# Kernel optimization log

Measured on AMD Instinct MI355X. Metric: run time of the kernel, lower is better.

Reference implementation:

```python
import jax, jax.numpy as jnp
import numpy as np

B = 65536      # bs * n_agents
N_AL = 9       # allies
N_EN = 10      # enemies
D_OWN = 96     # wrapped own obs dim (own + id + compact last action)
D_AL = 64      # ally feature dim
D_EN = 65      # enemy feature dim (+1 attack flag)
H = 4          # heads
A = 32         # attn_embed_dim per head
D = 32         # entity_embed_dim per head


def setup_inputs() -> dict:
    key = jax.random.key(0)
    ks = jax.random.split(key, 16)
    s = lambda fan_in: 1.0 / np.sqrt(fan_in)
    return {
        "own_obs": jax.random.normal(ks[0], (B, D_OWN), jnp.float32),
        "ally_feats": jax.random.normal(ks[1], (B, N_AL, D_AL), jnp.float32),
        "enemy_feats": jax.random.normal(ks[2], (B, N_EN, D_EN), jnp.float32),
        "Wq": jax.random.normal(ks[3], (D_OWN, A * H), jnp.float32) * s(D_OWN),
        "bq": jnp.zeros((A * H,), jnp.float32),
        "Wak": jax.random.normal(ks[4], (D_AL, A * H), jnp.float32) * s(D_AL),
        "bak": jnp.zeros((A * H,), jnp.float32),
        "Wav": jax.random.normal(ks[5], (D_AL, D * H), jnp.float32) * s(D_AL),
        "bav": jnp.zeros((D * H,), jnp.float32),
        "Wek": jax.random.normal(ks[6], (D_EN, A * H), jnp.float32) * s(D_EN),
        "bek": jnp.zeros((A * H,), jnp.float32),
        "Wev": jax.random.normal(ks[7], (D_EN, D * H), jnp.float32) * s(D_EN),
        "bev": jnp.zeros((D * H,), jnp.float32),
        "Wown": jax.random.normal(ks[8], (D_OWN, D * H), jnp.float32) * s(D_OWN),
        "bown": jnp.zeros((D * H,), jnp.float32),
    }


def _mha(q, k, v):
    # q: [B,H,A], k: [B,E,H,A], v: [B,E,H,D] -> [B, H*D]
    scale = jnp.asarray(1.0 / np.sqrt(A), q.dtype)
    energy = jnp.einsum("bha,beha->bhe", q, k) * scale
    score = jax.nn.softmax(energy, axis=-1)
    out = jnp.einsum("bhe,behd->bhd", score, v)
    return out.reshape(out.shape[0], H * D)


def reference(own_obs, ally_feats, enemy_feats, Wq, bq, Wak, bak, Wav, bav,
              Wek, bek, Wev, bev, Wown, bown):
    own_feature = own_obs @ Wown + bown                                   # [B, H*D]
    q = (own_obs @ Wq + bq).reshape(B, H, A)                              # [B,H,A]
    ally_k = (ally_feats @ Wak + bak).reshape(B, N_AL, H, A)
    ally_v = (ally_feats @ Wav + bav).reshape(B, N_AL, H, D)
    enemy_k = (enemy_feats @ Wek + bek).reshape(B, N_EN, H, A)
    enemy_v = (enemy_feats @ Wev + bev).reshape(B, N_EN, H, D)
    ally_feature = _mha(q, ally_k, ally_v)                                # [B, H*D]
    enemy_feature = _mha(q, enemy_k, enemy_v)                             # [B, H*D]
    attn_feature = jnp.concatenate([own_feature, ally_feature, enemy_feature], axis=-1)
    return attn_feature                                                   # [B, 3*H*D]
```

## Files before the change

kernel.cpp:

```cpp
#include <hip/hip_runtime.h>
#include <hip/hip_bf16.h>
#include <stdint.h>

#define N_AL 9
#define N_EN 10
#define D_OWN 96
#define D_AL 64
#define D_EN 65
#define BROWS 65536

#define WS_P0 0
#define WS_B0 49152
#define WS_P1 50176
#define WS_P2 87040
#define REGION 36864

#define QSCALE (0.17677669529663688f * 1.4426950408889634f)

typedef __attribute__((ext_vector_type(8))) short short8;
typedef __attribute__((ext_vector_type(4))) float f32x4;
typedef __attribute__((ext_vector_type(4), aligned(4))) float f32x4u;
typedef __attribute__((address_space(1))) const unsigned guint;
typedef __attribute__((address_space(3))) unsigned luint;

static __device__ __forceinline__ unsigned cvtpk(float lo, float hi) {
    unsigned r;
    asm("v_cvt_pk_bf16_f32 %0, %1, %2" : "=v"(r) : "v"(lo), "v"(hi));
    return r;
}
static __device__ __forceinline__ float bflo(unsigned u) { return __builtin_bit_cast(float, u << 16); }
static __device__ __forceinline__ float bfhi(unsigned u) { return __builtin_bit_cast(float, u & 0xffff0000u); }

static __device__ __forceinline__ short8 pack8(f32x4 a, f32x4 b) {
    union { unsigned u[4]; short8 s; } t;
    t.u[0] = cvtpk(a[0], a[1]); t.u[1] = cvtpk(a[2], a[3]);
    t.u[2] = cvtpk(b[0], b[1]); t.u[3] = cvtpk(b[2], b[3]);
    return t.s;
}
static __device__ __forceinline__ short f2bf1(float x) { return (short)(cvtpk(x, 0.0f) & 0xffffu); }

template <int CTRL>
static __device__ __forceinline__ float dpp_mov(float x) {
    return __builtin_bit_cast(float,
        __builtin_amdgcn_update_dpp(0, __builtin_bit_cast(int, x), CTRL, 0xf, 0xf, true));
}
static __device__ __forceinline__ float reduce16(float x) {
    x += dpp_mov<0xB1>(x);
    x += dpp_mov<0x4E>(x);
    x += dpp_mov<0x141>(x);
    x += dpp_mov<0x140>(x);
    return x;
}

__global__ void pack_weights(const float* __restrict__ Wq,  const float* __restrict__ bq,
                             const float* __restrict__ Wak, const float* __restrict__ Wav,
                             const float* __restrict__ bav, const float* __restrict__ Wek,
                             const float* __restrict__ Wev, const float* __restrict__ bev,
                             const float* __restrict__ Wown,const float* __restrict__ bown,
                             char* __restrict__ ws)
{
    int id = blockIdx.x * 256 + threadIdx.x;
    if (id < 7168) {
        const float *W0, *W1; int KS; short* dst; int f; bool isP0 = false;
        if (id < 3072)      { W0 = Wq;  W1 = Wown; KS = 3; dst = (short*)(ws + WS_P0); f = id; isP0 = true; }
        else if (id < 5120) { W0 = Wak; W1 = Wav;  KS = 2; dst = (short*)(ws + WS_P1); f = id - 3072; }
        else                { W0 = Wek; W1 = Wev;  KS = 2; dst = (short*)(ws + WS_P2); f = id - 5120; }
        int lane = f & 63, ks = (f >> 6) % KS, tile = f / (KS * 64);
        int col = tile * 16 + (lane & 15), k0 = ks * 32 + (lane >> 4) * 8;
        const float* W = (col < 128) ? W0 : W1;
        float scl = (isP0 && col < 128) ? QSCALE : 1.0f;
        int c = col & 127;
        short8 v;
        #pragma unroll
        for (int i = 0; i < 8; ++i) v[i] = f2bf1(W[(k0 + i) * 128 + c] * scl);
        *(short8*)(dst + (size_t)f * 8) = v;
    } else if (id < 7936) {
        int j = id - 7168;
        float* b0  = (float*)(ws + WS_B0);
        float* bV1 = (float*)(ws + WS_P1 + 32768);
        float* w64 = (float*)(ws + WS_P2 + 32768);
        float* bV2 = (float*)(ws + WS_P2 + 33792);
        if      (j < 128) b0[j] = bq[j] * QSCALE;
        else if (j < 256) b0[j] = bown[j - 128];
        else if (j < 384) w64[j - 256] = Wek[64 * 128 + (j - 256)];
        else if (j < 512) w64[j - 256] = Wev[64 * 128 + (j - 384)];
        else if (j < 640) bV1[j - 512] = bav[j - 512];
        else              bV2[j - 640] = bev[j - 640];
    }
}

static __device__ __forceinline__ void stage36(const char* src, char* smem, int wid, int lane) {
    #pragma unroll
    for (int c = 0; c < 9; ++c) {
        int off = (wid * 9 + c) * 1024;
        __builtin_amdgcn_global_load_lds((guint*)(src + off + lane * 16),
                                         (luint*)(smem + off), 16, 0, 0);
    }
}

static __device__ __forceinline__ void loadAllyRaw(const float* __restrict__ ally,
                                                   int arow, int kgrp, int e, f32x4* v) {
    const float* ap = ally + ((size_t)arow * N_AL + e) * D_AL + kgrp * 8;
    v[0] = *(const f32x4*)(ap);
    v[1] = *(const f32x4*)(ap + 4);
    v[2] = *(const f32x4*)(ap + 32);
    v[3] = *(const f32x4*)(ap + 36);
}

static __device__ __forceinline__ void loadEnemyRaw(const float* __restrict__ enemy,
                                                    int arow, int row0, int kgrp, int e,
                                                    f32x4* v, float* x64) {
    const float* ap = enemy + ((size_t)arow * N_EN + e) * D_EN + kgrp * 8;
    v[0] = *(const f32x4u*)(ap);
    v[1] = *(const f32x4u*)(ap + 4);
    v[2] = *(const f32x4u*)(ap + 32);
    v[3] = *(const f32x4u*)(ap + 36);
    #pragma unroll
    for (int r = 0; r < 4; ++r)
        x64[r] = enemy[((size_t)(row0 + kgrp * 4 + r) * N_EN + e) * D_EN + 64];
}

template <bool X64>
static __device__ __forceinline__ void entity_step(
    const short8* afr, const float* x64, const unsigned* qq,
    float (&accn)[2][4][4], float (&accd4)[4], const float (&hm)[4],
    const short* bpk, const float* w64lds, int lane)
{
    const int lrow = lane & 15;
    #pragma unroll
    for (int hp = 0; hp < 2; ++hp) {
        f32x4 acc4[4];
        #pragma unroll
        for (int j = 0; j < 4; ++j) {
            if (X64) {
                float w = w64lds[(4 * hp + j) * 16 + lrow];
                #pragma unroll
                for (int r = 0; r < 4; ++r) acc4[j][r] = x64[r] * w;
            } else {
                #pragma unroll
                for (int r = 0; r < 4; ++r) acc4[j][r] = 0.0f;
            }
        }
        #pragma unroll
        for (int ks = 0; ks < 2; ++ks)
            #pragma unroll
            for (int j = 0; j < 4; ++j) {
                short8 bfr = *(const short8*)(bpk + (size_t)(((4 * hp + j) * 2 + ks) * 64 + lane) * 8);
                acc4[j] = __builtin_amdgcn_mfma_f32_16x16x32_bf16(afr[ks], bfr, acc4[j], 0, 0, 0);
            }
        float p0[4], p1[4];
        #pragma unroll
        for (int r = 0; r < 4; ++r) { p0[r] = 0.0f; p1[r] = 0.0f; }
        #pragma unroll
        for (int j = 0; j < 4; ++j) {
            int t = 4 * hp + j;
            float* pp = (j < 2) ? p0 : p1;
            #pragma unroll
            for (int pr = 0; pr < 2; ++pr) {
                unsigned u = qq[t * 2 + pr];
                pp[2 * pr]     += bflo(u) * acc4[j][2 * pr];
                pp[2 * pr + 1] += bfhi(u) * acc4[j][2 * pr + 1];
            }
        }
        float s0[4], s1[4];
        #pragma unroll
        for (int r = 0; r < 4; ++r) {
            s0[r] = __builtin_amdgcn_exp2f(reduce16(p0[r]));
            s1[r] = __builtin_amdgcn_exp2f(reduce16(p1[r]));
            accd4[r] += hm[2 * hp] * s0[r] + hm[2 * hp + 1] * s1[r];
        }
        #pragma unroll
        for (int j = 0; j < 4; ++j) {
            if (X64) {
                float w = w64lds[128 + (4 * hp + j) * 16 + lrow];
                #pragma unroll
                for (int r = 0; r < 4; ++r) acc4[j][r] = x64[r] * w;
            } else {
                #pragma unroll
                for (int r = 0; r < 4; ++r) acc4[j][r] = 0.0f;
            }
        }
        #pragma unroll
        for (int ks = 0; ks < 2; ++ks)
            #pragma unroll
            for (int j = 0; j < 4; ++j) {
                short8 bfr = *(const short8*)(bpk + (size_t)(((8 + 4 * hp + j) * 2 + ks) * 64 + lane) * 8);
                acc4[j] = __builtin_amdgcn_mfma_f32_16x16x32_bf16(afr[ks], bfr, acc4[j], 0, 0, 0);
            }
        #pragma unroll
        for (int j = 0; j < 4; ++j) {
            const float* s = (j < 2) ? s0 : s1;
            #pragma unroll
            for (int r = 0; r < 4; ++r) accn[hp][j][r] += s[r] * acc4[j][r];
        }
    }
}

static __device__ __forceinline__ void write_attn(float* __restrict__ out, int row0, int kgrp,
                                                  int lrow, int coloff,
                                                  const float (&accn)[2][4][4],
                                                  const float (&accd4)[4],
                                                  const float* bVlds)
{
    float inv[4][4];
    #pragma unroll
    for (int r = 0; r < 4; ++r) {
        inv[0][r] = __builtin_amdgcn_rcpf(dpp_mov<0x00>(accd4[r]));
        inv[1][r] = __builtin_amdgcn_rcpf(dpp_mov<0x55>(accd4[r]));
        inv[2][r] = __builtin_amdgcn_rcpf(dpp_mov<0xAA>(accd4[r]));
        inv[3][r] = __builtin_amdgcn_rcpf(dpp_mov<0xFF>(accd4[r]));
    }
    #pragma unroll
    for (int hp = 0; hp < 2; ++hp)
        #pragma unroll
        for (int j = 0; j < 4; ++j) {
            int col = (4 * hp + j) * 16 + lrow;
            float bb = bVlds[col];
            #pragma unroll
            for (int r = 0; r < 4; ++r)
                out[(size_t)(row0 + kgrp * 4 + r) * 384 + coloff + col] =
                    accn[hp][j][r] * inv[2 * hp + (j >> 1)][r] + bb;
        }
}

__global__ __launch_bounds__(256, 4)
void TrSFRNNAgent_fused(const float* __restrict__ own,
                        const float* __restrict__ ally,
                        const float* __restrict__ enemy,
                        const char* __restrict__ ws,
                        float* __restrict__ out)
{
    __shared__ __align__(16) char smem[REGION];
    const int tid = threadIdx.x, lane = tid & 63, wid = tid >> 6;
    const int row0 = blockIdx.x * 64 + wid * 16;
    const int lrow = lane & 15, kgrp = lane >> 4;
    const int arow = row0 + lrow;
    float hm[4];
    #pragma unroll
    for (int h = 0; h < 4; ++h) hm[h] = ((lane & 3) == h) ? 1.0f : 0.0f;

    stage36(ws + WS_P1, smem, wid, lane);

    f32x4 prefA[4];
    loadAllyRaw(ally, arow, kgrp, 0, prefA);

    unsigned qq[16];
    {
        short8 afr0[3];
        {
            const float* ap = own + (size_t)arow * D_OWN + kgrp * 8;
            #pragma unroll
            for (int ks = 0; ks < 3; ++ks) {
                f32x4 a = *(const f32x4*)(ap + ks * 32);
                f32x4 b = *(const f32x4*)(ap + ks * 32 + 4);
                afr0[ks] = pack8(a, b);
            }
        }
        const short* bp0 = (const short*)(ws + WS_P0);
        const float* b0  = (const float*)(ws + WS_B0);
        #pragma unroll
        for (int pass = 0; pass < 2; ++pass) {
            f32x4 acc[8];
            #pragma unroll
            for (int t = 0; t < 8; ++t)
                #pragma unroll
                for (int r = 0; r < 4; ++r) acc[t][r] = 0.0f;
            #pragma unroll
            for (int ks = 0; ks < 3; ++ks)
                #pragma unroll
                for (int t = 0; t < 8; ++t) {
                    short8 bfr = *(const short8*)(bp0 + (size_t)(((pass * 8 + t) * 3 + ks) * 64 + lane) * 8);
                    acc[t] = __builtin_amdgcn_mfma_f32_16x16x32_bf16(afr0[ks], bfr, acc[t], 0, 0, 0);
                }
            if (pass == 0) {
                #pragma unroll
                for (int t = 0; t < 8; ++t) {
                    float bb = b0[t * 16 + lrow];
                    qq[t * 2]     = cvtpk(acc[t][0] + bb, acc[t][1] + bb);
                    qq[t * 2 + 1] = cvtpk(acc[t][2] + bb, acc[t][3] + bb);
                }
            } else {
                #pragma unroll
                for (int t = 0; t < 8; ++t) {
                    float bb = b0[128 + t * 16 + lrow];
                    #pragma unroll
                    for (int r = 0; r < 4; ++r)
                        out[(size_t)(row0 + kgrp * 4 + r) * 384 + t * 16 + lrow] = acc[t][r] + bb;
                }
            }
        }
    }
    __syncthreads();

    f32x4 prefE[4]; float x64e[4];
    {
        float accn[2][4][4] = {{{0}}}; float accd4[4] = {0, 0, 0, 0};
        #pragma unroll 1
        for (int e = 0; e < N_AL; ++e) {
            short8 afr[2];
            afr[0] = pack8(prefA[0], prefA[1]);
            afr[1] = pack8(prefA[2], prefA[3]);
            if (e + 1 < N_AL) loadAllyRaw(ally, arow, kgrp, e + 1, prefA);
            entity_step<false>(afr, nullptr, qq, accn, accd4, hm, (const short*)smem, nullptr, lane);
        }
        loadEnemyRaw(enemy, arow, row0, kgrp, 0, prefE, x64e);
        write_attn(out, row0, kgrp, lrow, 128, accn, accd4, (const float*)(smem + 32768));
    }
    __syncthreads();
    stage36(ws + WS_P2, smem, wid, lane);
    __syncthreads();

    {
        const float* w64lds = (const float*)(smem + 32768);
        float accn[2][4][4] = {{{0}}}; float accd4[4] = {0, 0, 0, 0};
        #pragma unroll 1
        for (int e = 0; e < N_EN; ++e) {
            short8 afr[2];
            afr[0] = pack8(prefE[0], prefE[1]);
            afr[1] = pack8(prefE[2], prefE[3]);
            float xc[4];
            #pragma unroll
            for (int r = 0; r < 4; ++r) xc[r] = x64e[r];
            if (e + 1 < N_EN) loadEnemyRaw(enemy, arow, row0, kgrp, e + 1, prefE, x64e);
            entity_step<true>(afr, xc, qq, accn, accd4, hm, (const short*)smem, w64lds, lane);
        }
        write_attn(out, row0, kgrp, lrow, 256, accn, accd4, (const float*)(smem + 33792));
    }
}

extern "C" void kernel_launch(void* const* d_in, const int* in_sizes, int n_in,
                              void* d_out, int out_size, void* d_ws, size_t ws_size,
                              hipStream_t stream)
{
    (void)in_sizes; (void)n_in; (void)out_size; (void)ws_size;
    const float* own   = (const float*)d_in[0];
    const float* ally  = (const float*)d_in[1];
    const float* enemy = (const float*)d_in[2];
    const float* Wq    = (const float*)d_in[3];
    const float* bq    = (const float*)d_in[4];
    const float* Wak   = (const float*)d_in[5];
    const float* Wav   = (const float*)d_in[7];
    const float* bav   = (const float*)d_in[8];
    const float* Wek   = (const float*)d_in[9];
    const float* Wev   = (const float*)d_in[11];
    const float* bev   = (const float*)d_in[12];
    const float* Wown  = (const float*)d_in[13];
    const float* bown  = (const float*)d_in[14];

    pack_weights<<<31, 256, 0, stream>>>(Wq, bq, Wak, Wav, bav, Wek, Wev, bev, Wown, bown,
                                         (char*)d_ws);
    TrSFRNNAgent_fused<<<BROWS / 64, 256, 0, stream>>>(own, ally, enemy,
                                                       (const char*)d_ws, (float*)d_out);
}
```

Measured before the change: 153.1 us.

## Hold K/V weight fragments in registers instead of staging through LDS

Removes the LDS staging of the ally and enemy K/V weight fragments and their block barriers. Each wave now loads all 32 bf16 B-fragments straight into registers once per phase and reuses them across every entity. The rank-1 term from the 65th enemy feature in the V projection is pulled out of the per-entity loop. It becomes a softmax-weighted scalar sum applied once at output time. Launch bounds drop from 4 to 2 blocks per SM so the larger register footprint fits, which trades occupancy for fewer LDS reads and syncs.

```diff
diff --git a/kernel.cpp b/kernel.cpp
--- a/kernel.cpp
+++ b/kernel.cpp
@@ -13,15 +13,12 @@
 #define WS_B0 49152
 #define WS_P1 50176
 #define WS_P2 87040
-#define REGION 36864
 
 #define QSCALE (0.17677669529663688f * 1.4426950408889634f)
 
 typedef __attribute__((ext_vector_type(8))) short short8;
 typedef __attribute__((ext_vector_type(4))) float f32x4;
 typedef __attribute__((ext_vector_type(4), aligned(4))) float f32x4u;
-typedef __attribute__((address_space(1))) const unsigned guint;
-typedef __attribute__((address_space(3))) unsigned luint;
 
 static __device__ __forceinline__ unsigned cvtpk(float lo, float hi) {
     unsigned r;
@@ -89,15 +86,6 @@
     }
 }
 
-static __device__ __forceinline__ void stage36(const char* src, char* smem, int wid, int lane) {
-    #pragma unroll
-    for (int c = 0; c < 9; ++c) {
-        int off = (wid * 9 + c) * 1024;
-        __builtin_amdgcn_global_load_lds((guint*)(src + off + lane * 16),
-                                         (luint*)(smem + off), 16, 0, 0);
-    }
-}
-
 static __device__ __forceinline__ void loadAllyRaw(const float* __restrict__ ally,
                                                    int arow, int kgrp, int e, f32x4* v) {
     const float* ap = ally + ((size_t)arow * N_AL + e) * D_AL + kgrp * 8;
@@ -122,35 +110,39 @@
 
 template <bool X64>
 static __device__ __forceinline__ void entity_step(
-    const short8* afr, const float* x64, const unsigned* qq,
-    float (&accn)[2][4][4], float (&accd4)[4], const float (&hm)[4],
-    const short* bpk, const float* w64lds, int lane)
-{
-    const int lrow = lane & 15;
+    const short8 (&afr)[2], const short8 (&BK)[16], const short8 (&BV)[16],
+    const unsigned* qq, float (&accn)[2][4][4], float (&accd4)[4], float (&SX)[4],
+    const float* x64, const float* w64K, int lane3)
+{
     #pragma unroll
     for (int hp = 0; hp < 2; ++hp) {
-        f32x4 acc4[4];
+        f32x4 kacc[4], vacc[4];
         #pragma unroll
         for (int j = 0; j < 4; ++j) {
             if (X64) {
-                float w = w64lds[(4 * hp + j) * 16 + lrow];
-                #pragma unroll
-                for (int r = 0; r < 4; ++r) acc4[j][r] = x64[r] * w;
+                float w = w64K[4 * hp + j];
+                #pragma unroll
+                for (int r = 0; r < 4; ++r) kacc[j][r] = x64[r] * w;
             } else {
                 #pragma unroll
-                for (int r = 0; r < 4; ++r) acc4[j][r] = 0.0f;
+                for (int r = 0; r < 4; ++r) kacc[j][r] = 0.0f;
             }
         }
         #pragma unroll
         for (int ks = 0; ks < 2; ++ks)
             #pragma unroll
-            for (int j = 0; j < 4; ++j) {
-                short8 bfr = *(const short8*)(bpk + (size_t)(((4 * hp + j) * 2 + ks) * 64 + lane) * 8);
-                acc4[j] = __builtin_amdgcn_mfma_f32_16x16x32_bf16(afr[ks], bfr, acc4[j], 0, 0, 0);
-            }
-        float p0[4], p1[4];
-        #pragma unroll
-        for (int r = 0; r < 4; ++r) { p0[r] = 0.0f; p1[r] = 0.0f; }
+            for (int j = 0; j < 4; ++j)
+                kacc[j] = __builtin_amdgcn_mfma_f32_16x16x32_bf16(afr[ks], BK[(4 * hp + j) * 2 + ks], kacc[j], 0, 0, 0);
+        #pragma unroll
+        for (int j = 0; j < 4; ++j)
+            #pragma unroll
+            for (int r = 0; r < 4; ++r) vacc[j][r] = 0.0f;
+        #pragma unroll
+        for (int ks = 0; ks < 2; ++ks)
+            #pragma unroll
+            for (int j = 0; j < 4; ++j)
+                vacc[j] = __builtin_amdgcn_mfma_f32_16x16x32_bf16(afr[ks], BV[(4 * hp + j) * 2 + ks], vacc[j], 0, 0, 0);
+        float p0[4] = {0, 0, 0, 0}, p1[4] = {0, 0, 0, 0};
         #pragma unroll
         for (int j = 0; j < 4; ++j) {
             int t = 4 * hp + j;
@@ -158,8 +150,8 @@
             #pragma unroll
             for (int pr = 0; pr < 2; ++pr) {
                 unsigned u = qq[t * 2 + pr];
-                pp[2 * pr]     += bflo(u) * acc4[j][2 * pr];
-                pp[2 * pr + 1] += bfhi(u) * acc4[j][2 * pr + 1];
+                pp[2 * pr]     += bflo(u) * kacc[j][2 * pr];
+                pp[2 * pr + 1] += bfhi(u) * kacc[j][2 * pr + 1];
             }
         }
         float s0[4], s1[4];
@@ -167,40 +159,27 @@
         for (int r = 0; r < 4; ++r) {
             s0[r] = __builtin_amdgcn_exp2f(reduce16(p0[r]));
             s1[r] = __builtin_amdgcn_exp2f(reduce16(p1[r]));
-            accd4[r] += hm[2 * hp] * s0[r] + hm[2 * hp + 1] * s1[r];
-        }
-        #pragma unroll
-        for (int j = 0; j < 4; ++j) {
-            if (X64) {
-                float w = w64lds[128 + (4 * hp + j) * 16 + lrow];
-                #pragma unroll
-                for (int r = 0; r < 4; ++r) acc4[j][r] = x64[r] * w;
-            } else {
-                #pragma unroll
-                for (int r = 0; r < 4; ++r) acc4[j][r] = 0.0f;
-            }
-        }
-        #pragma unroll
-        for (int ks = 0; ks < 2; ++ks)
-            #pragma unroll
-            for (int j = 0; j < 4; ++j) {
-                short8 bfr = *(const short8*)(bpk + (size_t)(((8 + 4 * hp + j) * 2 + ks) * 64 + lane) * 8);
-                acc4[j] = __builtin_amdgcn_mfma_f32_16x16x32_bf16(afr[ks], bfr, acc4[j], 0, 0, 0);
-            }
+            accd4[r] += (lane3 == 2 * hp ? s0[r] : 0.0f) + (lane3 == 2 * hp + 1 ? s1[r] : 0.0f);
+            if (X64)
+                SX[r] += (lane3 == 2 * hp ? s0[r] * x64[r] : 0.0f)
+                       + (lane3 == 2 * hp + 1 ? s1[r] * x64[r] : 0.0f);
+        }
         #pragma unroll
         for (int j = 0; j < 4; ++j) {
             const float* s = (j < 2) ? s0 : s1;
             #pragma unroll
-            for (int r = 0; r < 4; ++r) accn[hp][j][r] += s[r] * acc4[j][r];
-        }
-    }
-}
-
+            for (int r = 0; r < 4; ++r) accn[hp][j][r] += s[r] * vacc[j][r];
+        }
+    }
+}
+
+template <bool X64>
 static __device__ __forceinline__ void write_attn(float* __restrict__ out, int row0, int kgrp,
                                                   int lrow, int coloff,
                                                   const float (&accn)[2][4][4],
-                                                  const float (&accd4)[4],
-                                                  const float* bVlds)
+                                                  const float (&accd4)[4], const float (&SX)[4],
+                                                  const float* __restrict__ bV,
+                                                  const float* __restrict__ w64V)
 {
     float inv[4][4];
     #pragma unroll
@@ -210,36 +189,44 @@
         inv[2][r] = __builtin_amdgcn_rcpf(dpp_mov<0xAA>(accd4[r]));
         inv[3][r] = __builtin_amdgcn_rcpf(dpp_mov<0xFF>(accd4[r]));
     }
+    float sxh[4][4];
+    if (X64) {
+        #pragma unroll
+        for (int r = 0; r < 4; ++r) {
+            sxh[0][r] = dpp_mov<0x00>(SX[r]);
+            sxh[1][r] = dpp_mov<0x55>(SX[r]);
+            sxh[2][r] = dpp_mov<0xAA>(SX[r]);
+            sxh[3][r] = dpp_mov<0xFF>(SX[r]);
+        }
+    }
     #pragma unroll
     for (int hp = 0; hp < 2; ++hp)
         #pragma unroll
         for (int j = 0; j < 4; ++j) {
             int col = (4 * hp + j) * 16 + lrow;
-            float bb = bVlds[col];
-            #pragma unroll
-            for (int r = 0; r < 4; ++r)
-                out[(size_t)(row0 + kgrp * 4 + r) * 384 + coloff + col] =
-                    accn[hp][j][r] * inv[2 * hp + (j >> 1)][r] + bb;
-        }
-}
-
-__global__ __launch_bounds__(256, 4)
+            int h = 2 * hp + (j >> 1);
+            float bb = bV[col];
+            float wv = X64 ? w64V[col] : 0.0f;
+            #pragma unroll
+            for (int r = 0; r < 4; ++r) {
+                float a = accn[hp][j][r] + (X64 ? sxh[h][r] * wv : 0.0f);
+                out[(size_t)(row0 + kgrp * 4 + r) * 384 + coloff + col] = a * inv[h][r] + bb;
+            }
+        }
+}
+
+__global__ __launch_bounds__(256, 2)
 void TrSFRNNAgent_fused(const float* __restrict__ own,
                         const float* __restrict__ ally,
                         const float* __restrict__ enemy,
                         const char* __restrict__ ws,
                         float* __restrict__ out)
 {
-    __shared__ __align__(16) char smem[REGION];
     const int tid = threadIdx.x, lane = tid & 63, wid = tid >> 6;
     const int row0 = blockIdx.x * 64 + wid * 16;
     const int lrow = lane & 15, kgrp = lane >> 4;
     const int arow = row0 + lrow;
-    float hm[4];
-    #pragma unroll
-    for (int h = 0; h < 4; ++h) hm[h] = ((lane & 3) == h) ? 1.0f : 0.0f;
-
-    stage36(ws + WS_P1, smem, wid, lane);
+    const int lane3 = lane & 3;
 
     f32x4 prefA[4];
     loadAllyRaw(ally, arow, kgrp, 0, prefA);
@@ -290,10 +277,18 @@
             }
         }
     }
-    __syncthreads();
+
+    short8 BK[16], BV[16];
+    float SX[4] = {0, 0, 0, 0};
 
     f32x4 prefE[4]; float x64e[4];
     {
+        const short* bp = (const short*)(ws + WS_P1);
+        #pragma unroll
+        for (int f = 0; f < 16; ++f) BK[f] = *(const short8*)(bp + (size_t)(f * 64 + lane) * 8);
+        #pragma unroll
+        for (int f = 0; f < 16; ++f) BV[f] = *(const short8*)(bp + (size_t)((16 + f) * 64 + lane) * 8);
+
         float accn[2][4][4] = {{{0}}}; float accd4[4] = {0, 0, 0, 0};
         #pragma unroll 1
         for (int e = 0; e < N_AL; ++e) {
@@ -301,17 +296,24 @@
             afr[0] = pack8(prefA[0], prefA[1]);
             afr[1] = pack8(prefA[2], prefA[3]);
             if (e + 1 < N_AL) loadAllyRaw(ally, arow, kgrp, e + 1, prefA);
-            entity_step<false>(afr, nullptr, qq, accn, accd4, hm, (const short*)smem, nullptr, lane);
+            entity_step<false>(afr, BK, BV, qq, accn, accd4, SX, nullptr, nullptr, lane3);
         }
         loadEnemyRaw(enemy, arow, row0, kgrp, 0, prefE, x64e);
-        write_attn(out, row0, kgrp, lrow, 128, accn, accd4, (const float*)(smem + 32768));
-    }
-    __syncthreads();
-    stage36(ws + WS_P2, smem, wid, lane);
-    __syncthreads();
+        write_attn<false>(out, row0, kgrp, lrow, 128, accn, accd4, SX,
+                          (const float*)(ws + WS_P1 + 32768), nullptr);
+    }
 
     {
-        const float* w64lds = (const float*)(smem + 32768);
+        const short* bp = (const short*)(ws + WS_P2);
+        #pragma unroll
+        for (int f = 0; f < 16; ++f) BK[f] = *(const short8*)(bp + (size_t)(f * 64 + lane) * 8);
+        #pragma unroll
+        for (int f = 0; f < 16; ++f) BV[f] = *(const short8*)(bp + (size_t)((16 + f) * 64 + lane) * 8);
+        const float* w64base = (const float*)(ws + WS_P2 + 32768);
+        float w64K[8];
+        #pragma unroll
+        for (int t = 0; t < 8; ++t) w64K[t] = w64base[t * 16 + lrow];
+
         float accn[2][4][4] = {{{0}}}; float accd4[4] = {0, 0, 0, 0};
         #pragma unroll 1
         for (int e = 0; e < N_EN; ++e) {
@@ -322,9 +324,10 @@
             #pragma unroll
             for (int r = 0; r < 4; ++r) xc[r] = x64e[r];
             if (e + 1 < N_EN) loadEnemyRaw(enemy, arow, row0, kgrp, e + 1, prefE, x64e);
-            entity_step<true>(afr, xc, qq, accn, accd4, hm, (const short*)smem, w64lds, lane);
-        }
-        write_attn(out, row0, kgrp, lrow, 256, accn, accd4, (const float*)(smem + 33792));
+            entity_step<true>(afr, BK, BV, qq, accn, accd4, SX, xc, w64K, lane3);
+        }
+        write_attn<true>(out, row0, kgrp, lrow, 256, accn, accd4, SX,
+                         (const float*)(ws + WS_P2 + 33792), w64base + 128);
     }
 }
 
```

New measurement: 270.4 us. 1.77x slower.
